# Kernel optimization log

Measured on AMD Instinct MI355X. Metric: run time of the kernel, lower is better.

Reference implementation:

```python
import jax, jax.numpy as jnp
import numpy as np

E_QUBITS = 8  # embedding dim == number of qubits


def _iqp_amplitudes(x):
    """Statevector amplitudes of qml.IQPEmbedding(x) applied to |0..0>.

    x: [..., E] real. Returns [..., 2^E] complex64.
    Circuit: H on all wires, RZ(x_i) on wire i, MultiRZ(x_i*x_j) on all pairs i<j.
    For basis state z with signs s_i = (-1)^{z_i}:
      amp(z) = 2^{-E/2} * exp(i * phi(z)),
      phi(z) = -1/2 * sum_i x_i s_i - 1/2 * sum_{i<j} x_i x_j s_i s_j
             = -L/2 - (L^2 - ||x||^2)/4,  with L = sum_i x_i s_i.
    """
    E = x.shape[-1]
    z = jnp.arange(2 ** E)
    bits = (z[:, None] >> jnp.arange(E)[None, :]) & 1          # [2^E, E]
    s = (1.0 - 2.0 * bits).astype(x.dtype)                      # (-1)^{z_i}
    L = x @ s.T                                                 # [..., 2^E]
    sq = jnp.sum(x * x, axis=-1, keepdims=True)                 # ||x||^2
    phase = -0.5 * L - 0.25 * (L * L - sq)
    return jnp.exp(1j * phase) * (2.0 ** (-E / 2.0))            # complex64


def setup_inputs() -> dict:
    key = jax.random.key(0)
    kq, kk, kv = jax.random.split(key, 3)
    B, S, E = 16, 1024, E_QUBITS
    return {
        "Q": jax.random.normal(kq, (B, S, E), dtype=jnp.float32),
        "K": jax.random.normal(kk, (B, S, E), dtype=jnp.float32),
        "V": jax.random.normal(kv, (B, S, E), dtype=jnp.float32),
    }


def reference(Q, K, V):
    # Pure-state amplitudes for every token (IQP embedding). [B,S,2^E] complex
    aq = _iqp_amplitudes(Q)
    ak = _iqp_amplitudes(K)
    # Fidelity of pure states: |<psi_q|psi_k>|^2, batched Gram matrix.
    ip = jnp.einsum("bid,bjd->bij", jnp.conj(aq), ak)          # [B,S,S] complex
    fid = jnp.real(ip * jnp.conj(ip))                           # [B,S,S] float32
    attn = 2.0 * fid - 1.0
    return jnp.einsum("bij,bje->bie", attn, V)                  # [B,S,E]
```

## Files before the change

kernel.cpp:

```cpp
#include <hip/hip_runtime.h>
#include <hip/hip_bf16.h>
#include <stdint.h>

#define NB 16
#define S_LEN 1024
#define E_Q 8

typedef float v4f __attribute__((ext_vector_type(4)));
typedef short v8s __attribute__((ext_vector_type(8)));
typedef int   v4i __attribute__((ext_vector_type(4)));

__global__ __launch_bounds__(256) void build_tables(
    const float* __restrict__ Q, const float* __restrict__ K,
    uint16_t* __restrict__ Aq, uint16_t* __restrict__ Kt)
{
    const float* X = blockIdx.y ? K : Q;
    uint16_t*   T  = blockIdx.y ? Kt : Aq;

    const int tok = blockIdx.x * 16 + (threadIdx.x >> 4);
    const int hi  = threadIdx.x & 15;
    const int zb  = hi * 16;

    const float* x = X + tok * E_Q;
    float xv[E_Q]; float sq = 0.f;
#pragma unroll
    for (int i = 0; i < E_Q; ++i) { xv[i] = x[i]; sq += xv[i] * xv[i]; }
    const float qsq = 0.25f * sq;

    float L = xv[0] + xv[1] + xv[2] + xv[3];
#pragma unroll
    for (int i = 4; i < 8; ++i) L += ((hi >> (i - 4)) & 1) ? -xv[i] : xv[i];

    __align__(16) uint16_t cb[16];
    __align__(16) uint16_t sb[16];

    {
        const float phi = fmaf(-0.25f, L * L, fmaf(-0.5f, L, qsq));
        float s, c; __sincosf(phi, &s, &c);
        __hip_bfloat16 cbf = __float2bfloat16(c), sbf = __float2bfloat16(s);
        cb[0] = *(const uint16_t*)&cbf; sb[0] = *(const uint16_t*)&sbf;
    }
#pragma unroll
    for (int n = 1; n < 16; ++n) {
        const int g  = n ^ (n >> 1);
        const int gp = (n - 1) ^ ((n - 1) >> 1);
        const int t  = __builtin_ctz(g ^ gp);
        const float twox = 2.0f * xv[t];
        L = ((g >> t) & 1) ? (L - twox) : (L + twox);
        const float phi = fmaf(-0.25f, L * L, fmaf(-0.5f, L, qsq));
        float s, c; __sincosf(phi, &s, &c);
        __hip_bfloat16 cbf = __float2bfloat16(c), sbf = __float2bfloat16(s);
        cb[g] = *(const uint16_t*)&cbf; sb[g] = *(const uint16_t*)&sbf;
    }

    uint16_t* dst = T + (size_t)tok * 512;
    *(uint4*)(dst + zb)           = ((const uint4*)cb)[0];
    *(uint4*)(dst + zb + 8)       = ((const uint4*)cb)[1];
    *(uint4*)(dst + 256 + zb)     = ((const uint4*)sb)[0];
    *(uint4*)(dst + 256 + zb + 8) = ((const uint4*)sb)[1];
}

__global__ __launch_bounds__(256, 2) void qk_pv(
    const uint16_t* __restrict__ Aq, const uint16_t* __restrict__ Kt,
    const float* __restrict__ V, float* __restrict__ out)
{
    __shared__ __align__(16) char smem[65536];
    uint16_t* lAc = (uint16_t*)smem;
    uint16_t* lAs = (uint16_t*)(smem + 16384);
    uint16_t* lKc = (uint16_t*)(smem + 32768);
    uint16_t* lKs = (uint16_t*)(smem + 49152);
    uint16_t* lattn = (uint16_t*)smem;
    uint16_t* lVt   = (uint16_t*)(smem + 34816);

    const int jblk = blockIdx.x, iblk = blockIdx.y, b = blockIdx.z;
    const int tid  = threadIdx.x;
    const int lane = tid & 63, wv = tid >> 6;
    const int wm = wv >> 1, wn = wv & 1;
    const int r15 = lane & 15, qq = lane >> 4;

    int goff[4];
#pragma unroll
    for (int p = 0; p < 4; ++p) {
        const int f = p * 256 + tid;
        const int r = f >> 3, q = (f & 7) ^ (r & 7);
        goff[p] = r * 1024 + q * 16;
    }
    const int lbase = wv * 1024;

    const char* gA = (const char*)Aq + (size_t)(b * S_LEN + iblk * 128) * 1024;
    const char* gK = (const char*)Kt + (size_t)(b * S_LEN + jblk * 128) * 1024;

    const float4 vreg = ((const float4*)(V + ((size_t)b * S_LEN + jblk * 128) * E_Q))[tid];

    v4f accRe[4][4], accIm[4][4];
#pragma unroll
    for (int mi = 0; mi < 4; ++mi)
#pragma unroll
        for (int ni = 0; ni < 4; ++ni) {
            accRe[mi][ni] = (v4f)0.f;
            accIm[mi][ni] = (v4f)0.f;
        }

    for (int c = 0; c < 4; ++c) {
        __syncthreads();
        const int cbyte = c * 128;
#pragma unroll
        for (int p = 0; p < 4; ++p) {
            const int lo = p * 4096 + lbase;
            const char* sA = gA + cbyte + goff[p];
            const char* sK = gK + cbyte + goff[p];
            __builtin_amdgcn_global_load_lds(
                (const __attribute__((address_space(1))) void*)sA,
                (__attribute__((address_space(3))) void*)((char*)lAc + lo), 16, 0, 0);
            __builtin_amdgcn_global_load_lds(
                (const __attribute__((address_space(1))) void*)(sA + 512),
                (__attribute__((address_space(3))) void*)((char*)lAs + lo), 16, 0, 0);
            __builtin_amdgcn_global_load_lds(
                (const __attribute__((address_space(1))) void*)sK,
                (__attribute__((address_space(3))) void*)((char*)lKc + lo), 16, 0, 0);
            __builtin_amdgcn_global_load_lds(
                (const __attribute__((address_space(1))) void*)(sK + 512),
                (__attribute__((address_space(3))) void*)((char*)lKs + lo), 16, 0, 0);
        }
        __syncthreads();

#pragma unroll
        for (int ks2 = 0; ks2 < 2; ++ks2) {
            const int sl = ((ks2 * 4 + qq) ^ (r15 & 7)) * 8;
            v8s aqf[4], asf[4];
#pragma unroll
            for (int mi = 0; mi < 4; ++mi) {
                const int off = (wm * 64 + mi * 16 + r15) * 64 + sl;
                aqf[mi] = *(const v8s*)&lAc[off];
                asf[mi] = *(const v8s*)&lAs[off];
            }
#pragma unroll
            for (int ni = 0; ni < 4; ++ni) {
                const int koff = (wn * 64 + ni * 16 + r15) * 64 + sl;
                const v8s kc = *(const v8s*)&lKc[koff];
                const v8s ks = *(const v8s*)&lKs[koff];
                v4i kci = __builtin_bit_cast(v4i, kc);
                kci ^= (int)0x80008000;
                const v8s nkc = __builtin_bit_cast(v8s, kci);
#pragma unroll
                for (int mi = 0; mi < 4; ++mi) {
                    accRe[mi][ni] = __builtin_amdgcn_mfma_f32_16x16x32_bf16(aqf[mi], kc,  accRe[mi][ni], 0, 0, 0);
                    accRe[mi][ni] = __builtin_amdgcn_mfma_f32_16x16x32_bf16(asf[mi], ks,  accRe[mi][ni], 0, 0, 0);
                    accIm[mi][ni] = __builtin_amdgcn_mfma_f32_16x16x32_bf16(aqf[mi], ks,  accIm[mi][ni], 0, 0, 0);
                    accIm[mi][ni] = __builtin_amdgcn_mfma_f32_16x16x32_bf16(asf[mi], nkc, accIm[mi][ni], 0, 0, 0);
                }
            }
        }
    }

    __syncthreads();

    const float sc = 3.0517578125e-05f;
#pragma unroll
    for (int mi = 0; mi < 4; ++mi) {
#pragma unroll
        for (int ni = 0; ni < 4; ++ni) {
#pragma unroll
            for (int rg = 0; rg < 4; ++rg) {
                const float re = accRe[mi][ni][rg];
                const float im = accIm[mi][ni][rg];
                const float a  = fmaf(re * re + im * im, sc, -1.0f);
                const int row = wm * 64 + mi * 16 + qq * 4 + rg;
                const int col = wn * 64 + ni * 16 + r15;
                __hip_bfloat16 ab = __float2bfloat16(a);
                lattn[row * 136 + col] = *(const uint16_t*)&ab;
            }
        }
    }
    {
        const int j = tid >> 1, eh = (tid & 1) * 4;
        const float vv[4] = {vreg.x, vreg.y, vreg.z, vreg.w};
#pragma unroll
        for (int c2 = 0; c2 < 4; ++c2) {
            __hip_bfloat16 vb = __float2bfloat16(vv[c2]);
            lVt[(eh + c2) * 136 + j] = *(const uint16_t*)&vb;
        }
    }
    __syncthreads();

    v8s bfr[4];
#pragma unroll
    for (int ks3 = 0; ks3 < 4; ++ks3)
        bfr[ks3] = *(const v8s*)&lVt[r15 * 136 + ks3 * 32 + qq * 8];

    float* outb = out + (((size_t)b << 10) + iblk * 128) * E_Q;
#pragma unroll
    for (int mt = 0; mt < 2; ++mt) {
        const int rowbase = (wv * 2 + mt) * 16;
        v4f accO = (v4f)0.f;
#pragma unroll
        for (int ks3 = 0; ks3 < 4; ++ks3) {
            const v8s af = *(const v8s*)&lattn[(rowbase + r15) * 136 + ks3 * 32 + qq * 8];
            accO = __builtin_amdgcn_mfma_f32_16x16x32_bf16(af, bfr[ks3], accO, 0, 0, 0);
        }
        if (r15 < E_Q) {
            const int i0 = rowbase + qq * 4;
#pragma unroll
            for (int rg = 0; rg < 4; ++rg)
                atomicAdd(&outb[(i0 + rg) * E_Q + r15], accO[rg]);
        }
    }
}

extern "C" void kernel_launch(void* const* d_in, const int* in_sizes, int n_in,
                              void* d_out, int out_size, void* d_ws, size_t ws_size,
                              hipStream_t stream) {
    const float* Q = (const float*)d_in[0];
    const float* K = (const float*)d_in[1];
    const float* V = (const float*)d_in[2];
    float* out = (float*)d_out;

    uint16_t* Aq = (uint16_t*)d_ws;
    uint16_t* Kt = (uint16_t*)((char*)d_ws + (size_t)16 * 1024 * 1024);

    hipMemsetAsync(out, 0, (size_t)out_size * sizeof(float), stream);
    build_tables<<<dim3(NB * S_LEN / 16, 2), 256, 0, stream>>>(Q, K, Aq, Kt);
    qk_pv<<<dim3(S_LEN / 128, S_LEN / 128, NB), 256, 0, stream>>>(Aq, Kt, V, out);
}
```

Baseline: 102.4 us.

## Quantize IQP amplitude tables to int8 and use i8 MFMA for complex Gram

Amplitude cos/sin tables are now quantized to int8 (scaled by 127) instead of bf16. The K table stores cos, sin and -cos in one contiguous row, so each real and imaginary accumulator needs a single 16x16x64 i8 MFMA over a combined 512-wide K dimension rather than two bf16 MFMAs. This halves table bytes and MFMA instruction count and shrinks LDS use. The cost is coarser quantization of the amplitudes, which could hurt accuracy of the squared fidelity.

```diff
diff --git a/kernel.cpp b/kernel.cpp
--- a/kernel.cpp
+++ b/kernel.cpp
@@ -12,10 +12,10 @@
 
 __global__ __launch_bounds__(256) void build_tables(
     const float* __restrict__ Q, const float* __restrict__ K,
-    uint16_t* __restrict__ Aq, uint16_t* __restrict__ Kt)
+    int8_t* __restrict__ Aq, int8_t* __restrict__ Kt)
 {
-    const float* X = blockIdx.y ? K : Q;
-    uint16_t*   T  = blockIdx.y ? Kt : Aq;
+    const int which = blockIdx.y;
+    const float* X = which ? K : Q;
 
     const int tok = blockIdx.x * 16 + (threadIdx.x >> 4);
     const int hi  = threadIdx.x & 15;
@@ -31,14 +31,14 @@
 #pragma unroll
     for (int i = 4; i < 8; ++i) L += ((hi >> (i - 4)) & 1) ? -xv[i] : xv[i];
 
-    __align__(16) uint16_t cb[16];
-    __align__(16) uint16_t sb[16];
+    __align__(16) int8_t cb[16];
+    __align__(16) int8_t sb[16];
 
     {
         const float phi = fmaf(-0.25f, L * L, fmaf(-0.5f, L, qsq));
         float s, c; __sincosf(phi, &s, &c);
-        __hip_bfloat16 cbf = __float2bfloat16(c), sbf = __float2bfloat16(s);
-        cb[0] = *(const uint16_t*)&cbf; sb[0] = *(const uint16_t*)&sbf;
+        cb[0] = (int8_t)__float2int_rn(127.f * c);
+        sb[0] = (int8_t)__float2int_rn(127.f * s);
     }
 #pragma unroll
     for (int n = 1; n < 16; ++n) {
@@ -49,26 +49,33 @@
         L = ((g >> t) & 1) ? (L - twox) : (L + twox);
         const float phi = fmaf(-0.25f, L * L, fmaf(-0.5f, L, qsq));
         float s, c; __sincosf(phi, &s, &c);
-        __hip_bfloat16 cbf = __float2bfloat16(c), sbf = __float2bfloat16(s);
-        cb[g] = *(const uint16_t*)&cbf; sb[g] = *(const uint16_t*)&sbf;
-    }
-
-    uint16_t* dst = T + (size_t)tok * 512;
-    *(uint4*)(dst + zb)           = ((const uint4*)cb)[0];
-    *(uint4*)(dst + zb + 8)       = ((const uint4*)cb)[1];
-    *(uint4*)(dst + 256 + zb)     = ((const uint4*)sb)[0];
-    *(uint4*)(dst + 256 + zb + 8) = ((const uint4*)sb)[1];
+        cb[g] = (int8_t)__float2int_rn(127.f * c);
+        sb[g] = (int8_t)__float2int_rn(127.f * s);
+    }
+
+    if (which == 0) {
+        int8_t* dst = Aq + (size_t)tok * 512;
+        *(uint4*)(dst + zb)       = *(const uint4*)cb;
+        *(uint4*)(dst + 256 + zb) = *(const uint4*)sb;
+    } else {
+        __align__(16) int8_t nb[16];
+#pragma unroll
+        for (int i = 0; i < 16; ++i) nb[i] = (int8_t)(-cb[i]);
+        int8_t* dst = Kt + (size_t)tok * 768;
+        *(uint4*)(dst + zb)       = *(const uint4*)cb;
+        *(uint4*)(dst + 256 + zb) = *(const uint4*)sb;
+        *(uint4*)(dst + 512 + zb) = *(const uint4*)nb;
+    }
 }
 
 __global__ __launch_bounds__(256, 2) void qk_pv(
-    const uint16_t* __restrict__ Aq, const uint16_t* __restrict__ Kt,
+    const int8_t* __restrict__ Aq, const int8_t* __restrict__ Kt,
     const float* __restrict__ V, float* __restrict__ out)
 {
-    __shared__ __align__(16) char smem[65536];
-    uint16_t* lAc = (uint16_t*)smem;
-    uint16_t* lAs = (uint16_t*)(smem + 16384);
-    uint16_t* lKc = (uint16_t*)(smem + 32768);
-    uint16_t* lKs = (uint16_t*)(smem + 49152);
+    __shared__ __align__(16) char smem[49152];
+    int8_t* lA  = (int8_t*)smem;
+    int8_t* lK0 = (int8_t*)(smem + 16384);
+    int8_t* lK1 = (int8_t*)(smem + 32768);
     uint16_t* lattn = (uint16_t*)smem;
     uint16_t* lVt   = (uint16_t*)(smem + 34816);
 
@@ -78,27 +85,28 @@
     const int wm = wv >> 1, wn = wv & 1;
     const int r15 = lane & 15, qq = lane >> 4;
 
-    int goff[4];
+    int goffA[4], goffK[4];
 #pragma unroll
     for (int p = 0; p < 4; ++p) {
         const int f = p * 256 + tid;
         const int r = f >> 3, q = (f & 7) ^ (r & 7);
-        goff[p] = r * 1024 + q * 16;
+        goffA[p] = r * 512 + q * 16;
+        goffK[p] = r * 768 + q * 16;
     }
     const int lbase = wv * 1024;
 
-    const char* gA = (const char*)Aq + (size_t)(b * S_LEN + iblk * 128) * 1024;
-    const char* gK = (const char*)Kt + (size_t)(b * S_LEN + jblk * 128) * 1024;
+    const int8_t* gA = Aq + (size_t)(b * S_LEN + iblk * 128) * 512;
+    const int8_t* gK = Kt + (size_t)(b * S_LEN + jblk * 128) * 768;
 
     const float4 vreg = ((const float4*)(V + ((size_t)b * S_LEN + jblk * 128) * E_Q))[tid];
 
-    v4f accRe[4][4], accIm[4][4];
+    v4i accRe[4][4], accIm[4][4];
 #pragma unroll
     for (int mi = 0; mi < 4; ++mi)
 #pragma unroll
         for (int ni = 0; ni < 4; ++ni) {
-            accRe[mi][ni] = (v4f)0.f;
-            accIm[mi][ni] = (v4f)0.f;
+            accRe[mi][ni] = (v4i)0;
+            accIm[mi][ni] = (v4i)0;
         }
 
     for (int c = 0; c < 4; ++c) {
@@ -107,47 +115,36 @@
 #pragma unroll
         for (int p = 0; p < 4; ++p) {
             const int lo = p * 4096 + lbase;
-            const char* sA = gA + cbyte + goff[p];
-            const char* sK = gK + cbyte + goff[p];
             __builtin_amdgcn_global_load_lds(
-                (const __attribute__((address_space(1))) void*)sA,
-                (__attribute__((address_space(3))) void*)((char*)lAc + lo), 16, 0, 0);
+                (const __attribute__((address_space(1))) void*)(gA + cbyte + goffA[p]),
+                (__attribute__((address_space(3))) void*)(lA + lo), 16, 0, 0);
             __builtin_amdgcn_global_load_lds(
-                (const __attribute__((address_space(1))) void*)(sA + 512),
-                (__attribute__((address_space(3))) void*)((char*)lAs + lo), 16, 0, 0);
+                (const __attribute__((address_space(1))) void*)(gK + cbyte + goffK[p]),
+                (__attribute__((address_space(3))) void*)(lK0 + lo), 16, 0, 0);
             __builtin_amdgcn_global_load_lds(
-                (const __attribute__((address_space(1))) void*)sK,
-                (__attribute__((address_space(3))) void*)((char*)lKc + lo), 16, 0, 0);
-            __builtin_amdgcn_global_load_lds(
-                (const __attribute__((address_space(1))) void*)(sK + 512),
-                (__attribute__((address_space(3))) void*)((char*)lKs + lo), 16, 0, 0);
+                (const __attribute__((address_space(1))) void*)(gK + 256 + cbyte + goffK[p]),
+                (__attribute__((address_space(3))) void*)(lK1 + lo), 16, 0, 0);
         }
         __syncthreads();
 
 #pragma unroll
-        for (int ks2 = 0; ks2 < 2; ++ks2) {
-            const int sl = ((ks2 * 4 + qq) ^ (r15 & 7)) * 8;
-            v8s aqf[4], asf[4];
+        for (int w = 0; w < 2; ++w) {
+            v4i aF[4];
 #pragma unroll
             for (int mi = 0; mi < 4; ++mi) {
-                const int off = (wm * 64 + mi * 16 + r15) * 64 + sl;
-                aqf[mi] = *(const v8s*)&lAc[off];
-                asf[mi] = *(const v8s*)&lAs[off];
+                const int row = wm * 64 + mi * 16 + r15;
+                aF[mi] = *(const v4i*)&lA[row * 128 + (((w << 2) | qq) ^ (row & 7)) * 16];
             }
 #pragma unroll
             for (int ni = 0; ni < 4; ++ni) {
-                const int koff = (wn * 64 + ni * 16 + r15) * 64 + sl;
-                const v8s kc = *(const v8s*)&lKc[koff];
-                const v8s ks = *(const v8s*)&lKs[koff];
-                v4i kci = __builtin_bit_cast(v4i, kc);
-                kci ^= (int)0x80008000;
-                const v8s nkc = __builtin_bit_cast(v8s, kci);
+                const int rk  = wn * 64 + ni * 16 + r15;
+                const int off = rk * 128 + (((w << 2) | qq) ^ (rk & 7)) * 16;
+                const v4i k0 = *(const v4i*)&lK0[off];
+                const v4i k1 = *(const v4i*)&lK1[off];
 #pragma unroll
                 for (int mi = 0; mi < 4; ++mi) {
-                    accRe[mi][ni] = __builtin_amdgcn_mfma_f32_16x16x32_bf16(aqf[mi], kc,  accRe[mi][ni], 0, 0, 0);
-                    accRe[mi][ni] = __builtin_amdgcn_mfma_f32_16x16x32_bf16(asf[mi], ks,  accRe[mi][ni], 0, 0, 0);
-                    accIm[mi][ni] = __builtin_amdgcn_mfma_f32_16x16x32_bf16(aqf[mi], ks,  accIm[mi][ni], 0, 0, 0);
-                    accIm[mi][ni] = __builtin_amdgcn_mfma_f32_16x16x32_bf16(asf[mi], nkc, accIm[mi][ni], 0, 0, 0);
+                    accRe[mi][ni] = __builtin_amdgcn_mfma_i32_16x16x64_i8(aF[mi], k0, accRe[mi][ni], 0, 0, 0);
+                    accIm[mi][ni] = __builtin_amdgcn_mfma_i32_16x16x64_i8(aF[mi], k1, accIm[mi][ni], 0, 0, 0);
                 }
             }
         }
@@ -155,16 +152,16 @@
 
     __syncthreads();
 
-    const float sc = 3.0517578125e-05f;
+    const float sc2 = 3.0517578125e-05f / 260144641.0f;
 #pragma unroll
     for (int mi = 0; mi < 4; ++mi) {
 #pragma unroll
         for (int ni = 0; ni < 4; ++ni) {
 #pragma unroll
             for (int rg = 0; rg < 4; ++rg) {
-                const float re = accRe[mi][ni][rg];
-                const float im = accIm[mi][ni][rg];
-                const float a  = fmaf(re * re + im * im, sc, -1.0f);
+                const float rf  = (float)accRe[mi][ni][rg];
+                const float imf = (float)accIm[mi][ni][rg];
+                const float a   = fmaf(rf * rf + imf * imf, sc2, -1.0f);
                 const int row = wm * 64 + mi * 16 + qq * 4 + rg;
                 const int col = wn * 64 + ni * 16 + r15;
                 __hip_bfloat16 ab = __float2bfloat16(a);
@@ -215,8 +212,8 @@
     const float* V = (const float*)d_in[2];
     float* out = (float*)d_out;
 
-    uint16_t* Aq = (uint16_t*)d_ws;
-    uint16_t* Kt = (uint16_t*)((char*)d_ws + (size_t)16 * 1024 * 1024);
+    int8_t* Aq = (int8_t*)d_ws;
+    int8_t* Kt = (int8_t*)((char*)d_ws + (size_t)8 * 1024 * 1024);
 
     hipMemsetAsync(out, 0, (size_t)out_size * sizeof(float), stream);
     build_tables<<<dim3(NB * S_LEN / 16, 2), 256, 0, stream>>>(Q, K, Aq, Kt);
```

Measured after the change: 89.76 us. -12.3%, faster.
